# Kernel optimization log

Measured on AMD Instinct MI355X. Metric: run time of the kernel, lower is better.

## Reference

```python
import jax, jax.numpy as jnp
import numpy as np

H = 128; F = 64; G = 50; L = 4; CUT = 10.0
M = 256; K = 8; A = 32
N_TOPO = M * A; N = M * K * A; NCONF = M * K
E_CONF = N * 16; E_GRAPH = N_TOPO * 4
ATOM_TYPES = 100; BOND_TYPES = 10
OFFSETS = jnp.linspace(0.0, CUT, G)
GCOEFF = -0.5 / (CUT / (G - 1)) ** 2  # GaussianSmearing coeff
BN_EPS = 1e-5


def batchnorm(x, g, b):
    # BatchNorm1d in training mode: batch statistics over nodes
    mu = x.mean(0)
    var = ((x - mu) ** 2).mean(0)
    return (x - mu) * jax.lax.rsqrt(var + BN_EPS) * g + b


def setup_inputs():
    key = jax.random.key(0)
    ks = jax.random.split(key, 20)
    s = lambda k, shp: (jax.random.normal(k, shp) * 0.05).astype(jnp.float32)
    inp = {}
    inp["x_topo"] = jax.random.randint(ks[0], (N_TOPO,), 0, ATOM_TYPES)
    inp["pos"] = jax.random.normal(ks[1], (N, 3), dtype=jnp.float32) * 3.0
    inp["edge_index_conf"] = jax.random.randint(ks[2], (2, E_CONF), 0, N)
    inp["edge_index_graph"] = jax.random.randint(ks[3], (2, E_GRAPH), 0, N_TOPO)
    inp["edge_attr_graph"] = jax.random.randint(ks[4], (E_GRAPH,), 0, BOND_TYPES)
    # conf_node_batch: for molecule i, repeat arange(A)+i*A over K conformers
    cnb = (np.arange(M)[:, None, None] * A + np.broadcast_to(np.arange(A), (K, A))).reshape(-1)
    inp["conf_node_batch"] = jnp.asarray(cnb, dtype=jnp.int32)
    inp["pos_batch"] = jnp.repeat(jnp.arange(NCONF), A).astype(jnp.int32)
    inp["conf_batch"] = jnp.repeat(jnp.arange(M), K).astype(jnp.int32)
    # parameters
    inp["atom_emb"] = s(ks[5], (ATOM_TYPES, H))
    inp["cf_lin1_w"] = s(ks[6], (L, H, F))
    inp["cf_mlp_w1"] = s(ks[7], (L, G, F)); inp["cf_mlp_b1"] = jnp.zeros((L, F), jnp.float32)
    inp["cf_mlp_w2"] = s(ks[8], (L, F, F)); inp["cf_mlp_b2"] = jnp.zeros((L, F), jnp.float32)
    inp["cf_lin2_w"] = s(ks[9], (L, F, H)); inp["cf_lin2_b"] = jnp.zeros((L, H), jnp.float32)
    inp["lin_w"] = s(ks[10], (L, H, H)); inp["lin_b"] = jnp.zeros((L, H), jnp.float32)
    inp["bond_emb"] = s(ks[11], (L, BOND_TYPES, H))
    inp["gin_w1"] = s(ks[12], (L, H, H)); inp["gin_b1"] = jnp.zeros((L, H), jnp.float32)
    inp["gin_w2"] = s(ks[13], (L, H, H)); inp["gin_b2"] = jnp.zeros((L, H), jnp.float32)
    inp["gin_bn_g"] = jnp.ones((L, H), jnp.float32); inp["gin_bn_b"] = jnp.zeros((L, H), jnp.float32)
    inp["bn_g"] = jnp.ones((L, H), jnp.float32); inp["bn_b"] = jnp.zeros((L, H), jnp.float32)
    inp["gin_eps"] = jnp.zeros((L,), jnp.float32)
    inp["out_w1"] = s(ks[14], (H, H)); inp["out_b1"] = jnp.zeros((H,), jnp.float32)
    inp["out_w2"] = s(ks[15], (H, 1)); inp["out_b2"] = jnp.zeros((1,), jnp.float32)
    return inp


def _forward(x_topo, edge_index_conf, edge_index_graph, edge_attr_graph,
             conf_node_batch, pos_batch, conf_batch,
             pos, atom_emb, cf_lin1_w, cf_mlp_w1, cf_mlp_b1, cf_mlp_w2, cf_mlp_b2,
             cf_lin2_w, cf_lin2_b, lin_w, lin_b, bond_emb,
             gin_w1, gin_b1, gin_w2, gin_b2, gin_bn_g, gin_bn_b, bn_g, bn_b,
             gin_eps, out_w1, out_b1, out_w2, out_b2):
    # AtomEncoder on topo graph, broadcast to all conformers
    x = atom_emb[x_topo][conf_node_batch]                      # [N, H]
    row, col = edge_index_conf[0], edge_index_conf[1]
    d = pos[row] - pos[col]
    ew = jnp.sqrt(jnp.sum(d * d, axis=-1) + 1e-12)             # edge_weight_conf [E_conf]
    ea = jnp.exp(GCOEFF * (ew[:, None] - OFFSETS) ** 2)        # GaussianSmearing [E_conf, G]
    cwin = 0.5 * (jnp.cos(ew * jnp.pi / CUT) + 1.0)            # SchNet cosine cutoff
    gr, gc = edge_index_graph[0], edge_index_graph[1]
    for l in range(L):
        # CFConv branch (use_conf)
        Wf = (jax.nn.relu(ea @ cf_mlp_w1[l] + cf_mlp_b1[l]) @ cf_mlp_w2[l] + cf_mlp_b2[l]) * cwin[:, None]
        h = x @ cf_lin1_w[l]                                   # lin1, no bias
        agg = jax.ops.segment_sum(h[row] * Wf, col, num_segments=N)
        h = agg @ cf_lin2_w[l] + cf_lin2_b[l]                  # lin2
        h = jax.nn.relu(h)
        h = h @ lin_w[l] + lin_b[l]
        out = x + h                                            # residual
        # GIN branch on topo graph (use_graph)
        x_agg = jax.ops.segment_max(x, conf_node_batch, num_segments=N_TOPO)
        eemb = bond_emb[l][edge_attr_graph]                    # BondEncoder
        magg = jax.ops.segment_sum(jax.nn.relu(x_agg[gr] + eemb), gc, num_segments=N_TOPO)
        hg = (1.0 + gin_eps[l]) * x_agg + magg
        hg = jax.nn.relu(batchnorm(hg @ gin_w1[l] + gin_b1[l], gin_bn_g[l], gin_bn_b[l]))
        hg = hg @ gin_w2[l] + gin_b2[l]
        hg = batchnorm(hg, bn_g[l], bn_b[l])
        out = out + hg[conf_node_batch]
        x = jax.nn.relu(out)
    x = jax.ops.segment_max(x, pos_batch, num_segments=NCONF)  # pool atoms -> conformers
    x = jax.ops.segment_max(x, conf_batch, num_segments=M)     # pool conformers -> molecules
    x = jax.nn.relu(x @ out_w1 + out_b1) @ out_w2 + out_b2     # out_layer
    return x                                                   # training mode: no clamp


def reference(x_topo, pos, edge_index_conf, edge_index_graph, edge_attr_graph,
              conf_node_batch, pos_batch, conf_batch,
              atom_emb, cf_lin1_w, cf_mlp_w1, cf_mlp_b1, cf_mlp_w2, cf_mlp_b2,
              cf_lin2_w, cf_lin2_b, lin_w, lin_b, bond_emb,
              gin_w1, gin_b1, gin_w2, gin_b2, gin_bn_g, gin_bn_b, bn_g, bn_b,
              gin_eps, out_w1, out_b1, out_w2, out_b2):
    return _forward(x_topo, edge_index_conf, edge_index_graph, edge_attr_graph,
                    conf_node_batch, pos_batch, conf_batch,
                    pos, atom_emb, cf_lin1_w, cf_mlp_w1, cf_mlp_b1, cf_mlp_w2, cf_mlp_b2,
                    cf_lin2_w, cf_lin2_b, lin_w, lin_b, bond_emb,
                    gin_w1, gin_b1, gin_w2, gin_b2, gin_bn_g, gin_bn_b, bn_g, bn_b,
                    gin_eps, out_w1, out_b1, out_w2, out_b2)
```

## Files before the change

kernel.cpp:

```cpp
#include <hip/hip_runtime.h>
#include <hip/hip_bf16.h>

#define EC 1048576
#define NN 65536
#define NT 8192
#define MM 256
#define HH 128
#define FF 64
#define GG 50
#define EG 32768

#define TBL 2048
#define TBL_SHIFT 11
#define TRANGE 14.0f

#define CAP 32
#define OVF_CAP 8192
#define NEB (NN * 64 / 256)

#define SENT 0xFFE00000

constexpr float STEP = 10.0f / 49.0f;
constexpr float GC = -0.5f / (STEP * STEP);

typedef __attribute__((ext_vector_type(8))) short bf16x8;
typedef __attribute__((ext_vector_type(4))) float f32x4;

__device__ __forceinline__ ushort f2b(float v) {
    __hip_bfloat16 h = __float2bfloat16(v);
    return *(ushort*)&h;
}
__device__ __forceinline__ float b2f(ushort u) {
    return __uint_as_float(((unsigned)u) << 16);
}

__device__ __forceinline__ void prep_one(
    const float* __restrict__ W, ushort* __restrict__ Wf, int K, int N, int idx)
{
    int sz = K * N;
    int l = idx / sz;
    int t = idx - l * sz;
    int j = t & 7;
    int lane = (t >> 3) & 63;
    int rest = t >> 9;
    int KTl = K >> 5;
    int kt = rest % KTl;
    int nt = rest / KTl;
    int k = kt * 32 + (lane >> 4) * 8 + j;
    int n = nt * 16 + (lane & 15);
    Wf[idx] = f2b(W[(size_t)l * sz + (size_t)k * N + n]);
}

#define SETUP_B0 (EC / 256)
#define SETUP_B1 (SETUP_B0 + EG / 256)
#define SETUP_B2 (SETUP_B1 + NN * HH / 8 / 256)
#define SETUP_B3 (SETUP_B2 + 4 * TBL / 4)
#define SETUP_B4 (SETUP_B3 + 1024)
__global__ __launch_bounds__(256) void setup_kernel(
    const int* __restrict__ eic, const int* __restrict__ cnb,
    const int* __restrict__ eig, const float* __restrict__ pos,
    const float* __restrict__ emb, const int* __restrict__ xtopo,
    int* __restrict__ degC, ushort* __restrict__ xb,
    int* __restrict__ cntA, int* __restrict__ pay_pad,
    int* __restrict__ ovf_cnt, int2* __restrict__ ovf,
    const float* __restrict__ mw1, const float* __restrict__ mb1,
    const float* __restrict__ mw2, const float* __restrict__ mb2,
    float* __restrict__ table_all,
    const float* __restrict__ cf_lin1_w, const float* __restrict__ cf_lin2_w,
    const float* __restrict__ lin_w, const float* __restrict__ gin_w1,
    const float* __restrict__ gin_w2,
    ushort* __restrict__ w1f, ushort* __restrict__ w2f, ushort* __restrict__ wlf,
    ushort* __restrict__ gw1f, ushort* __restrict__ gw2f)
{
    int b = blockIdx.x, tid = threadIdx.x;
    if (b < SETUP_B0) {
        int e = b * 256 + tid;
        int r = eic[e], c = eic[EC + e];
        float dx = pos[r*3+0] - pos[c*3+0];
        float dy = pos[r*3+1] - pos[c*3+1];
        float dz = pos[r*3+2] - pos[c*3+2];
        float w = sqrtf(dx*dx + dy*dy + dz*dz + 1e-12f);
        float u = fminf(w * ((TBL - 1) / TRANGE), 2046.96875f);
        int pay = (((int)(u * 32.0f)) << 16) | (r & 0xFFFF);
        int slot = atomicAdd(&cntA[c], 1);
        if (slot < CAP) {
            __builtin_nontemporal_store(pay, &pay_pad[c * CAP + slot]);
        } else {
            int o = atomicAdd(ovf_cnt, 1);
            if (o < OVF_CAP) ovf[o] = make_int2(c, pay);
        }
    } else if (b < SETUP_B1) {
        atomicAdd(&degC[eig[EG + (b - SETUP_B0) * 256 + tid]], 1);
    } else if (b < SETUP_B2) {
        int idx = (b - SETUP_B1) * 256 + tid;
        int n = idx >> 4;
        int f8 = (idx & 15) << 3;
        const float* e = emb + (size_t)xtopo[cnb[n]] * HH + f8;
        float4 v0 = *(const float4*)e;
        float4 v1 = *(const float4*)(e + 4);
        ushort u[8] = {f2b(v0.x), f2b(v0.y), f2b(v0.z), f2b(v0.w),
                       f2b(v1.x), f2b(v1.y), f2b(v1.z), f2b(v1.w)};
        *(bf16x8*)(xb + ((size_t)idx << 3)) = *(const bf16x8*)u;
    } else if (b < SETUP_B3) {
        int entry = (b - SETUP_B2) * 4 + (tid >> 6);
        int l = entry >> TBL_SHIFT;
        int p = entry & (TBL - 1);
        int lane = tid & 63;
        int wv = tid >> 6;
        const float* w1 = mw1 + (size_t)l * GG * FF;
        const float* b1 = mb1 + (size_t)l * FF;
        const float* w2 = mw2 + (size_t)l * FF * FF;
        const float* b2 = mb2 + (size_t)l * FF;
        float w = p * (TRANGE / (TBL - 1));
        float t = b1[lane];
        for (int g = 0; g < GG; g++) {
            float d = w - g * STEP;
            float ea = __expf(GC * d * d);
            t = fmaf(ea, w1[g * 64 + lane], t);
        }
        __shared__ float ts[4][64];
        ts[wv][lane] = fmaxf(t, 0.f);
        __syncthreads();
        float wf = b2[lane];
        for (int i = 0; i < 64; i++)
            wf = fmaf(ts[wv][i], w2[i * 64 + lane], wf);
        float cw = 0.5f * (__cosf(w * (3.14159265358979323846f / 10.0f)) + 1.0f);
        table_all[((size_t)l * TBL + p) * 64 + lane] = wf * cw;
    } else {
        int pb = b - SETUP_B3;
        if (pb < 128)       prep_one(cf_lin1_w, w1f, HH, FF, pb * 256 + tid);
        else if (pb < 256)  prep_one(cf_lin2_w, w2f, FF, HH, (pb - 128) * 256 + tid);
        else if (pb < 512)  prep_one(lin_w, wlf, HH, HH, (pb - 256) * 256 + tid);
        else if (pb < 768)  prep_one(gin_w1, gw1f, HH, HH, (pb - 512) * 256 + tid);
        else                prep_one(gin_w2, gw2f, HH, HH, (pb - 768) * 256 + tid);
    }
}

__global__ __launch_bounds__(256) void scanC_kernel(
    const int* __restrict__ degC, int* __restrict__ offsC, int* __restrict__ curC)
{
    __shared__ int s[256];
    __shared__ int base;
    int tid = threadIdx.x;
    if (tid == 0) base = 0;
    __syncthreads();
    for (int c = 0; c < NT / 256; c++) {
        int v = degC[c * 256 + tid];
        s[tid] = v;
        __syncthreads();
        for (int off = 1; off < 256; off <<= 1) {
            int t = (tid >= off) ? s[tid - off] : 0;
            __syncthreads();
            s[tid] += t;
            __syncthreads();
        }
        int excl = s[tid] - v + base;
        offsC[c * 256 + tid] = excl;
        curC[c * 256 + tid] = excl;
        __syncthreads();
        if (tid == 255) base += s[255];
        __syncthreads();
    }
    if (tid == 0) offsC[NT] = EG;
}

__global__ __launch_bounds__(256) void scatter_graph_kernel(
    const int* __restrict__ eig, const int* __restrict__ eattr,
    int* __restrict__ curC, int2* __restrict__ gpay)
{
    int e = blockIdx.x * 256 + threadIdx.x;
    int p = atomicAdd(&curC[eig[EG + e]], 1);
    gpay[p] = make_int2(eig[e], eattr[e]);
}

__global__ __launch_bounds__(256) void pack_table_kernel(
    const float* __restrict__ table_all, ushort2* __restrict__ table2_all)
{
    int idx = blockIdx.x * 256 + threadIdx.x;
    int f = idx & 63;
    int rest = idx >> 6;
    int i = rest & (TBL - 1);
    int l = rest >> TBL_SHIFT;
    if (i == TBL - 1) {
        table2_all[idx] = make_ushort2(0, 0);
        return;
    }
    const float* T = table_all + ((size_t)l * TBL) * 64;
    float t0 = T[(size_t)i * 64 + f];
    float t1 = T[(size_t)(i + 1) * 64 + f];
    table2_all[idx] = make_ushort2(f2b(t0), f2b((t1 - t0) * 0.03125f));
}

__global__ __launch_bounds__(256) void gemm_bf16_kernel(
    const ushort* __restrict__ A, const ushort* __restrict__ Bf,
    ushort* __restrict__ Cb)
{
    int tid = threadIdx.x;
    int wave = tid >> 6, lane = tid & 63;
    int m0 = (blockIdx.x * 4 + wave) * 16;
    int arow = m0 + (lane & 15);
    int ak = (lane >> 4) * 8;
    bf16x8 a[4];
    const ushort* Ap = A + (size_t)arow * 128 + ak;
    #pragma unroll
    for (int kt = 0; kt < 4; kt++)
        a[kt] = *(const bf16x8*)(Ap + kt * 32);
    f32x4 acc[4];
    #pragma unroll
    for (int i = 0; i < 4; i++) acc[i] = (f32x4){0.f, 0.f, 0.f, 0.f};
    const ushort* Bp = Bf + (size_t)lane * 8;
    #pragma unroll
    for (int nt = 0; nt < 4; nt++)
        #pragma unroll
        for (int kt = 0; kt < 4; kt++) {
            bf16x8 b = *(const bf16x8*)(Bp + ((size_t)(nt * 4 + kt)) * 512);
            acc[nt] = __builtin_amdgcn_mfma_f32_16x16x32_bf16(a[kt], b, acc[nt], 0, 0, 0);
        }
    int col0 = lane & 15;
    int rbase = m0 + (lane >> 4) * 4;
    #pragma unroll
    for (int nt = 0; nt < 4; nt++) {
        int col = nt * 16 + col0;
        #pragma unroll
        for (int r = 0; r < 4; r++)
            Cb[(size_t)(rbase + r) * 64 + col] = f2b(acc[nt][r]);
    }
}

#define EDGE8(BASE) { \
    int pq[8]; \
    { int4 q0 = *(const int4*)(pp + BASE); \
      int4 q1 = *(const int4*)(pp + BASE + 4); \
      pq[0]=__builtin_amdgcn_readfirstlane(q0.x); \
      pq[1]=__builtin_amdgcn_readfirstlane(q0.y); \
      pq[2]=__builtin_amdgcn_readfirstlane(q0.z); \
      pq[3]=__builtin_amdgcn_readfirstlane(q0.w); \
      pq[4]=__builtin_amdgcn_readfirstlane(q1.x); \
      pq[5]=__builtin_amdgcn_readfirstlane(q1.y); \
      pq[6]=__builtin_amdgcn_readfirstlane(q1.z); \
      pq[7]=__builtin_amdgcn_readfirstlane(q1.w); } \
    float h[8]; \
    _Pragma("unroll") \
    for (int q = 0; q < 8; q++) \
        h[q] = b2f(*(const ushort*)(h1c + ((((unsigned)(pq[q] & 0xFFFF)) << 7) + lane2))); \
    unsigned tt[8]; \
    _Pragma("unroll") \
    for (int q = 0; q < 8; q++) \
        tt[q] = *(const unsigned*)(tbc + (((((unsigned)pq[q]) >> 21) << 8) + lane4)); \
    _Pragma("unroll") \
    for (int q = 0; q < 8; q++) { \
        float fr = (float)((unsigned)((pq[q] >> 16) & 31)); \
        float t0 = __uint_as_float(tt[q] << 16); \
        float dts = __uint_as_float(tt[q] & 0xFFFF0000u); \
        float wf = fmaf(dts, fr, t0); \
        if (q & 1) acc1 = fmaf(h[q], wf, acc1); else acc0 = fmaf(h[q], wf, acc0); \
    } }

__global__ __launch_bounds__(256) void edge_xagg_kernel(
    const int* __restrict__ cntA, const int* __restrict__ pay_pad,
    const int* __restrict__ ovf_cnt, const int2* __restrict__ ovf,
    const ushort2* __restrict__ table2, const ushort* __restrict__ h1b,
    ushort* __restrict__ aggb,
    const ushort* __restrict__ xb, ushort* __restrict__ xaggb)
{
    int tid = threadIdx.x;
    if (blockIdx.x < NEB) {
        int lane = tid & 63;
        int node = __builtin_amdgcn_readfirstlane((blockIdx.x * 256 + tid) >> 6);
        unsigned lane2 = (unsigned)lane * 2;
        unsigned lane4 = (unsigned)lane * 4;
        const char* h1c = (const char*)h1b;
        const char* tbc = (const char*)table2;
        int deg = cntA[node];
        int n1 = min(deg, CAP);
        const int* pp = pay_pad + (size_t)node * CAP;
        float acc0 = 0.f, acc1 = 0.f;
        EDGE8(0);
        if (n1 > 8) {
            EDGE8(8);
            if (n1 > 16) {
                EDGE8(16);
                if (n1 > 24) EDGE8(24);
            }
        }
        float acc = acc0 + acc1;
        if (deg > CAP) {
            int no = min(*ovf_cnt, OVF_CAP);
            for (int j = 0; j < no; j++) {
                int2 o = ovf[j];
                if (o.x == node) {
                    unsigned uf = (unsigned)o.y >> 16;
                    int i0 = uf >> 5;
                    float fr = (float)(uf & 31);
                    ushort2 ttv = table2[(size_t)i0 * 64 + lane];
                    acc = fmaf(b2f(h1b[(size_t)(o.y & 0xFFFF) * 64 + lane]),
                               fmaf(b2f(ttv.y), fr, b2f(ttv.x)), acc);
                }
            }
        }
        aggb[(size_t)node * 64 + lane] = f2b(acc);
    } else {
        int idx = (blockIdx.x - NEB) * 256 + tid;
        int tn = idx >> 7, f = idx & 127;
        int m = tn >> 5, a = tn & 31;
        const ushort* base = xb + ((size_t)((m << 8) + a)) * HH + f;
        float mx = -3.4e38f;
        #pragma unroll
        for (int k = 0; k < 8; k++)
            mx = fmaxf(mx, b2f(base[(size_t)(k << 5) * HH]));
        xaggb[idx] = f2b(mx);
    }
}

#define TSTR 136

__global__ __launch_bounds__(256) void gin_gemm1_kernel(
    const int* __restrict__ goffs, const int2* __restrict__ gpay,
    const ushort* __restrict__ xaggb, const float* __restrict__ bemb,
    const float* __restrict__ eps, const ushort* __restrict__ Bf,
    const float* __restrict__ bias, ushort* __restrict__ Cb,
    float* __restrict__ gsum, float* __restrict__ gsq)
{
    __shared__ ushort hg0s[64 * TSTR];
    __shared__ float ssum[128], ssq[128];
    int tid = threadIdx.x;
    if (tid < 128) { ssum[tid] = 0.f; ssq[tid] = 0.f; }
    {
        int row = tid >> 2;
        int fc = (tid & 3) * 32;
        int tn = blockIdx.x * 64 + row;
        float e1 = 1.0f + eps[0];
        float acc[32];
        const ushort* xo = xaggb + (size_t)tn * HH + fc;
        #pragma unroll
        for (int c = 0; c < 4; c++) {
            bf16x8 x = *(const bf16x8*)(xo + c * 8);
            #pragma unroll
            for (int j = 0; j < 8; j++)
                acc[c * 8 + j] = e1 * b2f((ushort)x[j]);
        }
        int beg = goffs[tn], end = goffs[tn + 1];
        for (int p = beg; p < end; p++) {
            int2 g = gpay[p];
            const ushort* xs = xaggb + (size_t)g.x * HH + fc;
            const float* bs = bemb + (size_t)g.y * HH + fc;
            #pragma unroll
            for (int c = 0; c < 4; c++) {
                bf16x8 x = *(const bf16x8*)(xs + c * 8);
                float4 b0 = *(const float4*)(bs + c * 8);
                float4 b1 = *(const float4*)(bs + c * 8 + 4);
                float bb[8] = {b0.x, b0.y, b0.z, b0.w, b1.x, b1.y, b1.z, b1.w};
                #pragma unroll
                for (int j = 0; j < 8; j++)
                    acc[c * 8 + j] += fmaxf(b2f((ushort)x[j]) + bb[j], 0.f);
            }
        }
        ushort* dst = hg0s + row * TSTR + fc;
        #pragma unroll
        for (int j = 0; j < 32; j++) dst[j] = f2b(acc[j]);
    }
    __syncthreads();
    int wave = tid >> 6, lane = tid & 63;
    int lm = lane & 15, lq = lane >> 4;
    int ak = lq * 8;
    bf16x8 a[4];
    #pragma unroll
    for (int kt = 0; kt < 4; kt++)
        a[kt] = *(const bf16x8*)&hg0s[(wave * 16 + lm) * TSTR + ak + kt * 32];
    f32x4 acc[8];
    #pragma unroll
    for (int i = 0; i < 8; i++) acc[i] = (f32x4){0.f, 0.f, 0.f, 0.f};
    const ushort* Bp = Bf + (size_t)lane * 8;
    #pragma unroll
    for (int nt = 0; nt < 8; nt++)
        #pragma unroll
        for (int kt = 0; kt < 4; kt++) {
            bf16x8 b = *(const bf16x8*)(Bp + ((size_t)(nt * 4 + kt)) * 512);
            acc[nt] = __builtin_amdgcn_mfma_f32_16x16x32_bf16(a[kt], b, acc[nt], 0, 0, 0);
        }
    int rbase = blockIdx.x * 64 + wave * 16 + lq * 4;
    #pragma unroll
    for (int nt = 0; nt < 8; nt++) {
        int col = nt * 16 + lm;
        float bs = bias[col];
        float ps = 0.f, pq = 0.f;
        #pragma unroll
        for (int r = 0; r < 4; r++) {
            float v = acc[nt][r] + bs;
            Cb[(size_t)(rbase + r) * 128 + col] = f2b(v);
            ps += v; pq += v * v;
        }
        atomicAdd(&ssum[col], ps);
        atomicAdd(&ssq[col], pq);
    }
    __syncthreads();
    if (tid < 128) {
        atomicAdd(&gsum[tid], ssum[tid]);
        atomicAdd(&gsq[tid], ssq[tid]);
    }
}

__global__ __launch_bounds__(256) void gemm_bn_stats_kernel(
    const ushort* __restrict__ Araw, const float* __restrict__ sum1,
    const float* __restrict__ sq1, const float* __restrict__ g1,
    const float* __restrict__ bb1, const ushort* __restrict__ Bf,
    const float* __restrict__ bias, ushort* __restrict__ Cb,
    float* __restrict__ gsum, float* __restrict__ gsq)
{
    __shared__ float ssum[128], ssq[128];
    int tid = threadIdx.x;
    if (tid < 128) { ssum[tid] = 0.f; ssq[tid] = 0.f; }
    __syncthreads();
    int wave = tid >> 6, lane = tid & 63;
    int m0 = (blockIdx.x * 4 + wave) * 16;
    int arow = m0 + (lane & 15);
    int ak = (lane >> 4) * 8;
    const float INV_NT = 1.0f / NT;
    bf16x8 a[4];
    const ushort* Ap = Araw + (size_t)arow * 128 + ak;
    #pragma unroll
    for (int kt = 0; kt < 4; kt++) {
        bf16x8 raw = *(const bf16x8*)(Ap + kt * 32);
        ushort ub[8];
        #pragma unroll
        for (int j = 0; j < 8; j++) {
            int k = ak + kt * 32 + j;
            float mu = sum1[k] * INV_NT;
            float var = sq1[k] * INV_NT - mu * mu;
            float inv = rsqrtf(var + 1e-5f);
            float w = fmaxf((b2f((ushort)raw[j]) - mu) * inv * g1[k] + bb1[k], 0.f);
            ub[j] = f2b(w);
        }
        a[kt] = *(bf16x8*)ub;
    }
    f32x4 acc[8];
    #pragma unroll
    for (int i = 0; i < 8; i++) acc[i] = (f32x4){0.f, 0.f, 0.f, 0.f};
    const ushort* Bp = Bf + (size_t)lane * 8;
    #pragma unroll
    for (int nt = 0; nt < 8; nt++)
        #pragma unroll
        for (int kt = 0; kt < 4; kt++) {
            bf16x8 b = *(const bf16x8*)(Bp + ((size_t)(nt * 4 + kt)) * 512);
            acc[nt] = __builtin_amdgcn_mfma_f32_16x16x32_bf16(a[kt], b, acc[nt], 0, 0, 0);
        }
    int col0 = lane & 15;
    int rbase = m0 + (lane >> 4) * 4;
    #pragma unroll
    for (int nt = 0; nt < 8; nt++) {
        int col = nt * 16 + col0;
        float bs = bias[col];
        float ps = 0.f, pq = 0.f;
        #pragma unroll
        for (int r = 0; r < 4; r++) {
            float v = acc[nt][r] + bs;
            Cb[(size_t)(rbase + r) * 128 + col] = f2b(v);
            ps += v; pq += v * v;
        }
        atomicAdd(&ssum[col], ps);
        atomicAdd(&ssq[col], pq);
    }
    __syncthreads();
    if (tid < 128) {
        atomicAdd(&gsum[tid], ssum[tid]);
        atomicAdd(&gsq[tid], ssq[tid]);
    }
}

__global__ __launch_bounds__(256) void fused_lin_kernel(
    const ushort* __restrict__ aggb, const ushort* __restrict__ w2,
    const float* __restrict__ b2, const ushort* __restrict__ w3,
    const float* __restrict__ b3, const ushort* __restrict__ hgBb,
    const float* __restrict__ sum2, const float* __restrict__ sq2,
    const float* __restrict__ g2, const float* __restrict__ bb2,
    const int* __restrict__ cnb, const ushort* __restrict__ w1n,
    ushort* __restrict__ xb, ushort* __restrict__ h1b)
{
    __shared__ ushort t1s[4][16 * TSTR];
    __shared__ ushort t2s[4][16 * TSTR];
    int tid = threadIdx.x;
    int wave = tid >> 6, lane = tid & 63;
    int m0 = (blockIdx.x * 4 + wave) * 16;
    int lm = lane & 15;
    int lq = lane >> 4;
    ushort* T1 = t1s[wave];
    ushort* T2 = t2s[wave];
    const float INV_NT = 1.0f / NT;

    const ushort* Ap = aggb + (size_t)(m0 + lm) * 64 + lq * 8;
    bf16x8 a1[2];
    a1[0] = *(const bf16x8*)(Ap);
    a1[1] = *(const bf16x8*)(Ap + 32);
    f32x4 acc[8];
    #pragma unroll
    for (int i = 0; i < 8; i++) acc[i] = (f32x4){0.f, 0.f, 0.f, 0.f};
    {
        const ushort* Bp = w2 + (size_t)lane * 8;
        #pragma unroll
        for (int nt = 0; nt < 8; nt++)
            #pragma unroll
            for (int kt = 0; kt < 2; kt++) {
                bf16x8 b = *(const bf16x8*)(Bp + ((size_t)(nt * 2 + kt)) * 512);
                acc[nt] = __builtin_amdgcn_mfma_f32_16x16x32_bf16(a1[kt], b, acc[nt], 0, 0, 0);
            }
    }
    #pragma unroll
    for (int nt = 0; nt < 8; nt++) {
        int col = nt * 16 + lm;
        float bs = b2[col];
        #pragma unroll
        for (int r = 0; r < 4; r++) {
            float v = fmaxf(acc[nt][r] + bs, 0.f);
            T1[(lq * 4 + r) * TSTR + col] = f2b(v);
        }
    }
    __syncthreads();

    bf16x8 a2[4];
    #pragma unroll
    for (int kt = 0; kt < 4; kt++)
        a2[kt] = *(const bf16x8*)&T1[lm * TSTR + kt * 32 + lq * 8];
    __syncthreads();
    #pragma unroll
    for (int i = 0; i < 4; i++) {
        int idx = i * 64 + lane;
        int row = idx >> 4, ch = idx & 15;
        bf16x8 v = *(const bf16x8*)(xb + (size_t)(m0 + row) * HH + ch * 8);
        *(bf16x8*)&T1[row * TSTR + ch * 8] = v;
    }
    #pragma unroll
    for (int i = 0; i < 8; i++) acc[i] = (f32x4){0.f, 0.f, 0.f, 0.f};
    {
        const ushort* Bp = w3 + (size_t)lane * 8;
        #pragma unroll
        for (int nt = 0; nt < 8; nt++)
            #pragma unroll
            for (int kt = 0; kt < 4; kt++) {
                bf16x8 b = *(const bf16x8*)(Bp + ((size_t)(nt * 4 + kt)) * 512);
                acc[nt] = __builtin_amdgcn_mfma_f32_16x16x32_bf16(a2[kt], b, acc[nt], 0, 0, 0);
            }
    }
    int rbase = m0 + lq * 4;
    int cn[4];
    #pragma unroll
    for (int r = 0; r < 4; r++) cn[r] = cnb[rbase + r];
    #pragma unroll
    for (int nt = 0; nt < 8; nt++) {
        int col = nt * 16 + lm;
        float bs = b3[col];
        float mu2 = sum2[col] * INV_NT;
        float var2 = sq2[col] * INV_NT - mu2 * mu2;
        float sc2 = rsqrtf(var2 + 1e-5f) * g2[col];
        float sh2 = bb2[col] - mu2 * sc2;
        #pragma unroll
        for (int r = 0; r < 4; r++) {
            float v = acc[nt][r] + bs;
            v += b2f(T1[(lq * 4 + r) * TSTR + col]);
            v = fmaf(b2f(hgBb[(size_t)cn[r] * HH + col]), sc2, v + sh2);
            v = fmaxf(v, 0.f);
            T2[(lq * 4 + r) * TSTR + col] = f2b(v);
        }
    }
    __syncthreads();
    #pragma unroll
    for (int i = 0; i < 4; i++) {
        int idx = i * 64 + lane;
        int row = idx >> 4, ch = idx & 15;
        bf16x8 v = *(const bf16x8*)&T2[row * TSTR + ch * 8];
        *(bf16x8*)(xb + (size_t)(m0 + row) * HH + ch * 8) = v;
    }
    if (!w1n) return;
    __syncthreads();

    bf16x8 a3[4];
    #pragma unroll
    for (int kt = 0; kt < 4; kt++)
        a3[kt] = *(const bf16x8*)&T2[lm * TSTR + kt * 32 + lq * 8];
    f32x4 acc3[4];
    #pragma unroll
    for (int i = 0; i < 4; i++) acc3[i] = (f32x4){0.f, 0.f, 0.f, 0.f};
    {
        const ushort* Bp = w1n + (size_t)lane * 8;
        #pragma unroll
        for (int nt = 0; nt < 4; nt++)
            #pragma unroll
            for (int kt = 0; kt < 4; kt++) {
                bf16x8 b = *(const bf16x8*)(Bp + ((size_t)(nt * 4 + kt)) * 512);
                acc3[nt] = __builtin_amdgcn_mfma_f32_16x16x32_bf16(a3[kt], b, acc3[nt], 0, 0, 0);
            }
    }
    #pragma unroll
    for (int nt = 0; nt < 4; nt++) {
        int col = nt * 16 + lm;
        #pragma unroll
        for (int r = 0; r < 4; r++)
            T1[(lq * 4 + r) * TSTR + col] = f2b(acc3[nt][r]);
    }
    __syncthreads();
    #pragma unroll
    for (int i = 0; i < 2; i++) {
        int idx = i * 64 + lane;
        int row = idx >> 3, ch = idx & 7;
        bf16x8 v = *(const bf16x8*)&T1[row * TSTR + ch * 8];
        *(bf16x8*)(h1b + (size_t)(m0 + row) * FF + ch * 8) = v;
    }
}

__global__ __launch_bounds__(128) void out_layer_kernel(
    const ushort* __restrict__ xb, const float* __restrict__ w1,
    const float* __restrict__ b1, const float* __restrict__ w2,
    const float* __restrict__ b2, float* __restrict__ out)
{
    int m = blockIdx.x, f = threadIdx.x;
    const ushort* base = xb + (size_t)m * 256 * HH + f;
    float mx = -3.4e38f;
    for (int r = 0; r < 256; r++)
        mx = fmaxf(mx, b2f(base[(size_t)r * HH]));
    __shared__ float xs[128];
    xs[f] = mx;
    __syncthreads();
    float acc = b1[f];
    for (int k = 0; k < 128; k++) acc = fmaf(xs[k], w1[k * HH + f], acc);
    acc = fmaxf(acc, 0.f) * w2[f];
    __shared__ float red[128];
    red[f] = acc;
    __syncthreads();
    for (int off = 64; off > 0; off >>= 1) {
        if (f < off) red[f] += red[f + off];
        __syncthreads();
    }
    if (f == 0) out[m] = red[0] + b2[0];
}

extern "C" void kernel_launch(void* const* d_in, const int* in_sizes, int n_in,
                              void* d_out, int out_size, void* d_ws, size_t ws_size,
                              hipStream_t stream)
{
    const int*   x_topo    = (const int*)d_in[0];
    const float* pos       = (const float*)d_in[1];
    const int*   eic       = (const int*)d_in[2];
    const int*   eig       = (const int*)d_in[3];
    const int*   eattr     = (const int*)d_in[4];
    const int*   cnb       = (const int*)d_in[5];
    const float* atom_emb  = (const float*)d_in[8];
    const float* cf_lin1_w = (const float*)d_in[9];
    const float* cf_mlp_w1 = (const float*)d_in[10];
    const float* cf_mlp_b1 = (const float*)d_in[11];
    const float* cf_mlp_w2 = (const float*)d_in[12];
    const float* cf_mlp_b2 = (const float*)d_in[13];
    const float* cf_lin2_w = (const float*)d_in[14];
    const float* cf_lin2_b = (const float*)d_in[15];
    const float* lin_w     = (const float*)d_in[16];
    const float* lin_b     = (const float*)d_in[17];
    const float* bond_emb  = (const float*)d_in[18];
    const float* gin_w1    = (const float*)d_in[19];
    const float* gin_b1    = (const float*)d_in[20];
    const float* gin_w2    = (const float*)d_in[21];
    const float* gin_b2    = (const float*)d_in[22];
    const float* gin_bn_g  = (const float*)d_in[23];
    const float* gin_bn_b  = (const float*)d_in[24];
    const float* bn_g      = (const float*)d_in[25];
    const float* bn_b      = (const float*)d_in[26];
    const float* gin_eps   = (const float*)d_in[27];
    const float* out_w1    = (const float*)d_in[28];
    const float* out_b1    = (const float*)d_in[29];
    const float* out_w2    = (const float*)d_in[30];
    const float* out_b2    = (const float*)d_in[31];
    float* out = (float*)d_out;

    char* wsb = (char*)d_ws;
    size_t off = 0;
    auto alloc = [&](size_t nbytes) -> void* {
        void* p = (void*)(wsb + off);
        off += (nbytes + 255) & ~(size_t)255;
        return p;
    };
    ushort* xb      = (ushort*)alloc((size_t)NN * HH * 2);
    ushort* h1b     = (ushort*)alloc((size_t)NN * FF * 2);
    ushort* aggb    = (ushort*)alloc((size_t)NN * FF * 2);
    ushort* xaggb   = (ushort*)alloc((size_t)NT * HH * 2);
    ushort* hgA     = (ushort*)alloc((size_t)NT * HH * 2);
    ushort* hgB     = (ushort*)alloc((size_t)NT * HH * 2);
    float*  table_all  = (float*)alloc((size_t)4 * TBL * 64 * 4);
    ushort2* table2_all = (ushort2*)alloc((size_t)4 * TBL * 64 * 4);
    float*  stats   = (float*)alloc((size_t)4 * 4 * 128 * 4);
    int*    cntA    = (int*)alloc((size_t)NN * 4);
    int*    degC    = (int*)alloc((size_t)NT * 4);
    int*    ovf_cnt = (int*)alloc(256);
    int*    offsC   = (int*)alloc((NT + 1) * 4);
    int*    curC    = (int*)alloc(NT * 4);
    int*    pay_pad = (int*)alloc((size_t)NN * CAP * 4);
    int2*   ovf     = (int2*)alloc((size_t)OVF_CAP * 8);
    int2*   gpay    = (int2*)alloc((size_t)EG * 8);
    ushort* w1f     = (ushort*)alloc((size_t)4 * HH * FF * 2);
    ushort* w2f     = (ushort*)alloc((size_t)4 * FF * HH * 2);
    ushort* wlf     = (ushort*)alloc((size_t)4 * HH * HH * 2);
    ushort* gw1f    = (ushort*)alloc((size_t)4 * HH * HH * 2);
    ushort* gw2f    = (ushort*)alloc((size_t)4 * HH * HH * 2);

    hipMemsetAsync(stats, 0,
        ((size_t)4 * 4 * 128 * 4 + 255 & ~(size_t)255) +
        ((size_t)NN * 4 + 255 & ~(size_t)255) +
        ((size_t)NT * 4 + 255 & ~(size_t)255) + 256, stream);
    hipMemsetD32Async((hipDeviceptr_t)pay_pad, SENT, (size_t)NN * CAP, stream);

    setup_kernel<<<SETUP_B4, 256, 0, stream>>>(
        eic, cnb, eig, pos, atom_emb, x_topo, degC, xb, cntA, pay_pad, ovf_cnt, ovf,
        cf_mlp_w1, cf_mlp_b1, cf_mlp_w2, cf_mlp_b2, table_all,
        cf_lin1_w, cf_lin2_w, lin_w, gin_w1, gin_w2, w1f, w2f, wlf, gw1f, gw2f);
    scanC_kernel<<<1, 256, 0, stream>>>(degC, offsC, curC);
    scatter_graph_kernel<<<EG / 256, 256, 0, stream>>>(eig, eattr, curC, gpay);
    pack_table_kernel<<<4 * TBL * 64 / 256, 256, 0, stream>>>(table_all, table2_all);

    gemm_bf16_kernel<<<NN / 64, 256, 0, stream>>>(xb, w1f, h1b);

    for (int l = 0; l < 4; l++) {
        const ushort2* table2 = table2_all + (size_t)l * TBL * 64;
        float* sum1 = stats + (size_t)l * 512;
        float* sq1  = sum1 + 128;
        float* sum2 = sum1 + 256;
        float* sq2  = sum1 + 384;
        edge_xagg_kernel<<<NEB + NT * HH / 256, 256, 0, stream>>>(
            cntA, pay_pad, ovf_cnt, ovf, table2, h1b, aggb, xb, xaggb);
        gin_gemm1_kernel<<<NT / 64, 256, 0, stream>>>(
            offsC, gpay, xaggb, bond_emb + (size_t)l * 10 * HH, gin_eps + l,
            gw1f + (size_t)l * HH * HH, gin_b1 + (size_t)l * HH, hgA, sum1, sq1);
        gemm_bn_stats_kernel<<<NT / 64, 256, 0, stream>>>(
            hgA, sum1, sq1, gin_bn_g + (size_t)l * HH, gin_bn_b + (size_t)l * HH,
            gw2f + (size_t)l * HH * HH, gin_b2 + (size_t)l * HH, hgB, sum2, sq2);
        fused_lin_kernel<<<NN / 64, 256, 0, stream>>>(
            aggb, w2f + (size_t)l * FF * HH, cf_lin2_b + (size_t)l * HH,
            wlf + (size_t)l * HH * HH, lin_b + (size_t)l * HH,
            hgB, sum2, sq2, bn_g + (size_t)l * HH, bn_b + (size_t)l * HH,
            cnb, (l < 3) ? (w1f + (size_t)(l + 1) * HH * FF) : nullptr,
            xb, h1b);
    }

    out_layer_kernel<<<MM, 128, 0, stream>>>(xb, out_w1, out_b1, out_w2, out_b2, out);
}
```

Measured before the change: 639.2 us.

## Replace graph CSR scan/scatter with padded bucket adjacency and merge setup launches

```diff
diff --git a/kernel.cpp b/kernel.cpp
--- a/kernel.cpp
+++ b/kernel.cpp
@@ -16,6 +16,8 @@
 
 #define CAP 32
 #define OVF_CAP 8192
+#define GCAP 32
+#define GOVF_CAP 1024
 #define NEB (NN * 64 / 256)
 
 #define SENT 0xFFE00000
@@ -58,11 +60,13 @@
 #define SETUP_B4 (SETUP_B3 + 1024)
 __global__ __launch_bounds__(256) void setup_kernel(
     const int* __restrict__ eic, const int* __restrict__ cnb,
-    const int* __restrict__ eig, const float* __restrict__ pos,
+    const int* __restrict__ eig, const int* __restrict__ eattr,
+    const float* __restrict__ pos,
     const float* __restrict__ emb, const int* __restrict__ xtopo,
-    int* __restrict__ degC, ushort* __restrict__ xb,
+    ushort* __restrict__ xb,
     int* __restrict__ cntA, int* __restrict__ pay_pad,
     int* __restrict__ ovf_cnt, int2* __restrict__ ovf,
+    int* __restrict__ gcnt, int2* __restrict__ gpay_pad, int4* __restrict__ govf,
     const float* __restrict__ mw1, const float* __restrict__ mb1,
     const float* __restrict__ mw2, const float* __restrict__ mb2,
     float* __restrict__ table_all,
@@ -84,13 +88,22 @@
         int pay = (((int)(u * 32.0f)) << 16) | (r & 0xFFFF);
         int slot = atomicAdd(&cntA[c], 1);
         if (slot < CAP) {
-            __builtin_nontemporal_store(pay, &pay_pad[c * CAP + slot]);
+            pay_pad[c * CAP + slot] = pay;
         } else {
-            int o = atomicAdd(ovf_cnt, 1);
+            int o = atomicAdd(&ovf_cnt[0], 1);
             if (o < OVF_CAP) ovf[o] = make_int2(c, pay);
         }
     } else if (b < SETUP_B1) {
-        atomicAdd(&degC[eig[EG + (b - SETUP_B0) * 256 + tid]], 1);
+        int e = (b - SETUP_B0) * 256 + tid;
+        int src = eig[e], dst = eig[EG + e];
+        int at = eattr[e];
+        int slot = atomicAdd(&gcnt[dst], 1);
+        if (slot < GCAP) {
+            gpay_pad[dst * GCAP + slot] = make_int2(src, at);
+        } else {
+            int o = atomicAdd(&ovf_cnt[1], 1);
+            if (o < GOVF_CAP) govf[o] = make_int4(dst, src, at, 0);
+        }
     } else if (b < SETUP_B2) {
         int idx = (b - SETUP_B1) * 256 + tid;
         int n = idx >> 4;
@@ -136,94 +149,58 @@
     }
 }
 
-__global__ __launch_bounds__(256) void scanC_kernel(
-    const int* __restrict__ degC, int* __restrict__ offsC, int* __restrict__ curC)
-{
-    __shared__ int s[256];
-    __shared__ int base;
-    int tid = threadIdx.x;
-    if (tid == 0) base = 0;
-    __syncthreads();
-    for (int c = 0; c < NT / 256; c++) {
-        int v = degC[c * 256 + tid];
-        s[tid] = v;
-        __syncthreads();
-        for (int off = 1; off < 256; off <<= 1) {
-            int t = (tid >= off) ? s[tid - off] : 0;
-            __syncthreads();
-            s[tid] += t;
-            __syncthreads();
-        }
-        int excl = s[tid] - v + base;
-        offsC[c * 256 + tid] = excl;
-        curC[c * 256 + tid] = excl;
-        __syncthreads();
-        if (tid == 255) base += s[255];
-        __syncthreads();
-    }
-    if (tid == 0) offsC[NT] = EG;
-}
-
-__global__ __launch_bounds__(256) void scatter_graph_kernel(
-    const int* __restrict__ eig, const int* __restrict__ eattr,
-    int* __restrict__ curC, int2* __restrict__ gpay)
-{
-    int e = blockIdx.x * 256 + threadIdx.x;
-    int p = atomicAdd(&curC[eig[EG + e]], 1);
-    gpay[p] = make_int2(eig[e], eattr[e]);
-}
-
-__global__ __launch_bounds__(256) void pack_table_kernel(
-    const float* __restrict__ table_all, ushort2* __restrict__ table2_all)
-{
-    int idx = blockIdx.x * 256 + threadIdx.x;
-    int f = idx & 63;
-    int rest = idx >> 6;
-    int i = rest & (TBL - 1);
-    int l = rest >> TBL_SHIFT;
-    if (i == TBL - 1) {
-        table2_all[idx] = make_ushort2(0, 0);
-        return;
-    }
-    const float* T = table_all + ((size_t)l * TBL) * 64;
-    float t0 = T[(size_t)i * 64 + f];
-    float t1 = T[(size_t)(i + 1) * 64 + f];
-    table2_all[idx] = make_ushort2(f2b(t0), f2b((t1 - t0) * 0.03125f));
-}
-
-__global__ __launch_bounds__(256) void gemm_bf16_kernel(
+#define S2_B0 (4 * TBL * 64 / 256)
+#define S2_B1 (S2_B0 + NN / 64)
+__global__ __launch_bounds__(256) void stage2_kernel(
+    const float* __restrict__ table_all, ushort2* __restrict__ table2_all,
     const ushort* __restrict__ A, const ushort* __restrict__ Bf,
     ushort* __restrict__ Cb)
 {
-    int tid = threadIdx.x;
-    int wave = tid >> 6, lane = tid & 63;
-    int m0 = (blockIdx.x * 4 + wave) * 16;
-    int arow = m0 + (lane & 15);
-    int ak = (lane >> 4) * 8;
-    bf16x8 a[4];
-    const ushort* Ap = A + (size_t)arow * 128 + ak;
-    #pragma unroll
-    for (int kt = 0; kt < 4; kt++)
-        a[kt] = *(const bf16x8*)(Ap + kt * 32);
-    f32x4 acc[4];
-    #pragma unroll
-    for (int i = 0; i < 4; i++) acc[i] = (f32x4){0.f, 0.f, 0.f, 0.f};
-    const ushort* Bp = Bf + (size_t)lane * 8;
-    #pragma unroll
-    for (int nt = 0; nt < 4; nt++)
-        #pragma unroll
-        for (int kt = 0; kt < 4; kt++) {
-            bf16x8 b = *(const bf16x8*)(Bp + ((size_t)(nt * 4 + kt)) * 512);
-            acc[nt] = __builtin_amdgcn_mfma_f32_16x16x32_bf16(a[kt], b, acc[nt], 0, 0, 0);
-        }
-    int col0 = lane & 15;
-    int rbase = m0 + (lane >> 4) * 4;
-    #pragma unroll
-    for (int nt = 0; nt < 4; nt++) {
-        int col = nt * 16 + col0;
-        #pragma unroll
-        for (int r = 0; r < 4; r++)
-            Cb[(size_t)(rbase + r) * 64 + col] = f2b(acc[nt][r]);
+    int b = blockIdx.x, tid = threadIdx.x;
+    if (b < S2_B0) {
+        int idx = b * 256 + tid;
+        int f = idx & 63;
+        int rest = idx >> 6;
+        int i = rest & (TBL - 1);
+        int l = rest >> TBL_SHIFT;
+        if (i == TBL - 1) {
+            table2_all[idx] = make_ushort2(0, 0);
+            return;
+        }
+        const float* T = table_all + ((size_t)l * TBL) * 64;
+        float t0 = T[(size_t)i * 64 + f];
+        float t1 = T[(size_t)(i + 1) * 64 + f];
+        table2_all[idx] = make_ushort2(f2b(t0), f2b((t1 - t0) * 0.03125f));
+    } else {
+        int wave = tid >> 6, lane = tid & 63;
+        int m0 = ((b - S2_B0) * 4 + wave) * 16;
+        int arow = m0 + (lane & 15);
+        int ak = (lane >> 4) * 8;
+        bf16x8 a[4];
+        const ushort* Ap = A + (size_t)arow * 128 + ak;
+        #pragma unroll
+        for (int kt = 0; kt < 4; kt++)
+            a[kt] = *(const bf16x8*)(Ap + kt * 32);
+        f32x4 acc[4];
+        #pragma unroll
+        for (int i = 0; i < 4; i++) acc[i] = (f32x4){0.f, 0.f, 0.f, 0.f};
+        const ushort* Bp = Bf + (size_t)lane * 8;
+        #pragma unroll
+        for (int nt = 0; nt < 4; nt++)
+            #pragma unroll
+            for (int kt = 0; kt < 4; kt++) {
+                bf16x8 bb = *(const bf16x8*)(Bp + ((size_t)(nt * 4 + kt)) * 512);
+                acc[nt] = __builtin_amdgcn_mfma_f32_16x16x32_bf16(a[kt], bb, acc[nt], 0, 0, 0);
+            }
+        int col0 = lane & 15;
+        int rbase = m0 + (lane >> 4) * 4;
+        #pragma unroll
+        for (int nt = 0; nt < 4; nt++) {
+            int col = nt * 16 + col0;
+            #pragma unroll
+            for (int r = 0; r < 4; r++)
+                Cb[(size_t)(rbase + r) * 64 + col] = f2b(acc[nt][r]);
+        }
     }
 }
 
@@ -285,7 +262,7 @@
         }
         float acc = acc0 + acc1;
         if (deg > CAP) {
-            int no = min(*ovf_cnt, OVF_CAP);
+            int no = min(ovf_cnt[0], OVF_CAP);
             for (int j = 0; j < no; j++) {
                 int2 o = ovf[j];
                 if (o.x == node) {
@@ -315,7 +292,8 @@
 #define TSTR 136
 
 __global__ __launch_bounds__(256) void gin_gemm1_kernel(
-    const int* __restrict__ goffs, const int2* __restrict__ gpay,
+    const int* __restrict__ gcnt, const int2* __restrict__ gpay_pad,
+    const int* __restrict__ ovf_cnt, const int4* __restrict__ govf,
     const ushort* __restrict__ xaggb, const float* __restrict__ bemb,
     const float* __restrict__ eps, const ushort* __restrict__ Bf,
     const float* __restrict__ bias, ushort* __restrict__ Cb,
@@ -339,9 +317,11 @@
             for (int j = 0; j < 8; j++)
                 acc[c * 8 + j] = e1 * b2f((ushort)x[j]);
         }
-        int beg = goffs[tn], end = goffs[tn + 1];
-        for (int p = beg; p < end; p++) {
-            int2 g = gpay[p];
+        int deg = gcnt[tn];
+        int gn = min(deg, GCAP);
+        const int2* gp = gpay_pad + (size_t)tn * GCAP;
+        for (int p = 0; p < gn; p++) {
+            int2 g = gp[p];
             const ushort* xs = xaggb + (size_t)g.x * HH + fc;
             const float* bs = bemb + (size_t)g.y * HH + fc;
             #pragma unroll
@@ -353,6 +333,26 @@
                 #pragma unroll
                 for (int j = 0; j < 8; j++)
                     acc[c * 8 + j] += fmaxf(b2f((ushort)x[j]) + bb[j], 0.f);
+            }
+        }
+        if (deg > GCAP) {
+            int no = min(ovf_cnt[1], GOVF_CAP);
+            for (int j2 = 0; j2 < no; j2++) {
+                int4 o = govf[j2];
+                if (o.x == tn) {
+                    const ushort* xs = xaggb + (size_t)o.y * HH + fc;
+                    const float* bs = bemb + (size_t)o.z * HH + fc;
+                    #pragma unroll
+                    for (int c = 0; c < 4; c++) {
+                        bf16x8 x = *(const bf16x8*)(xs + c * 8);
+                        float4 b0 = *(const float4*)(bs + c * 8);
+                        float4 b1 = *(const float4*)(bs + c * 8 + 4);
+                        float bb[8] = {b0.x, b0.y, b0.z, b0.w, b1.x, b1.y, b1.z, b1.w};
+                        #pragma unroll
+                        for (int j = 0; j < 8; j++)
+                            acc[c * 8 + j] += fmaxf(b2f((ushort)x[j]) + bb[j], 0.f);
+                    }
+                }
             }
         }
         ushort* dst = hg0s + row * TSTR + fc;
@@ -685,13 +685,12 @@
     ushort2* table2_all = (ushort2*)alloc((size_t)4 * TBL * 64 * 4);
     float*  stats   = (float*)alloc((size_t)4 * 4 * 128 * 4);
     int*    cntA    = (int*)alloc((size_t)NN * 4);
-    int*    degC    = (int*)alloc((size_t)NT * 4);
+    int*    gcnt    = (int*)alloc((size_t)NT * 4);
     int*    ovf_cnt = (int*)alloc(256);
-    int*    offsC   = (int*)alloc((NT + 1) * 4);
-    int*    curC    = (int*)alloc(NT * 4);
     int*    pay_pad = (int*)alloc((size_t)NN * CAP * 4);
     int2*   ovf     = (int2*)alloc((size_t)OVF_CAP * 8);
-    int2*   gpay    = (int2*)alloc((size_t)EG * 8);
+    int2*   gpay_pad = (int2*)alloc((size_t)NT * GCAP * 8);
+    int4*   govf    = (int4*)alloc((size_t)GOVF_CAP * 16);
     ushort* w1f     = (ushort*)alloc((size_t)4 * HH * FF * 2);
     ushort* w2f     = (ushort*)alloc((size_t)4 * FF * HH * 2);
     ushort* wlf     = (ushort*)alloc((size_t)4 * HH * HH * 2);
@@ -705,14 +704,11 @@
     hipMemsetD32Async((hipDeviceptr_t)pay_pad, SENT, (size_t)NN * CAP, stream);
 
     setup_kernel<<<SETUP_B4, 256, 0, stream>>>(
-        eic, cnb, eig, pos, atom_emb, x_topo, degC, xb, cntA, pay_pad, ovf_cnt, ovf,
+        eic, cnb, eig, eattr, pos, atom_emb, x_topo, xb,
+        cntA, pay_pad, ovf_cnt, ovf, gcnt, gpay_pad, govf,
         cf_mlp_w1, cf_mlp_b1, cf_mlp_w2, cf_mlp_b2, table_all,
         cf_lin1_w, cf_lin2_w, lin_w, gin_w1, gin_w2, w1f, w2f, wlf, gw1f, gw2f);
-    scanC_kernel<<<1, 256, 0, stream>>>(degC, offsC, curC);
-    scatter_graph_kernel<<<EG / 256, 256, 0, stream>>>(eig, eattr, curC, gpay);
-    pack_table_kernel<<<4 * TBL * 64 / 256, 256, 0, stream>>>(table_all, table2_all);
-
-    gemm_bf16_kernel<<<NN / 64, 256, 0, stream>>>(xb, w1f, h1b);
+    stage2_kernel<<<S2_B1, 256, 0, stream>>>(table_all, table2_all, xb, w1f, h1b);
 
     for (int l = 0; l < 4; l++) {
         const ushort2* table2 = table2_all + (size_t)l * TBL * 64;
@@ -723,7 +719,7 @@
         edge_xagg_kernel<<<NEB + NT * HH / 256, 256, 0, stream>>>(
             cntA, pay_pad, ovf_cnt, ovf, table2, h1b, aggb, xb, xaggb);
         gin_gemm1_kernel<<<NT / 64, 256, 0, stream>>>(
-            offsC, gpay, xaggb, bond_emb + (size_t)l * 10 * HH, gin_eps + l,
+            gcnt, gpay_pad, ovf_cnt, govf, xaggb, bond_emb + (size_t)l * 10 * HH, gin_eps + l,
             gw1f + (size_t)l * HH * HH, gin_b1 + (size_t)l * HH, hgA, sum1, sq1);
         gemm_bn_stats_kernel<<<NT / 64, 256, 0, stream>>>(
             hgA, sum1, sq1, gin_bn_g + (size_t)l * HH, gin_bn_b + (size_t)l * HH,
```

Result: faster. 589.1 us (-7.8%).
